# Kernel tuning notes

Hardware: AMD Instinct MI355X
Metric: run time of the kernel (lower is better)

The kernel has to match this reference:

```python
import jax, jax.numpy as jnp
import numpy as np

N, E, B, H, W = 2048, 65536, 4, 64, 64
D, ED, HID, ATT, STEPS = 128, 128, 256, 16, 4
NODE_IN, EDGE_IN = 256, 64


def setup_inputs() -> dict:
    key = jax.random.key(0)
    ks = jax.random.split(key, 24)
    p = lambda k, s: jax.random.normal(k, s, jnp.float32) * 0.05
    z = lambda n: jnp.zeros((n,), jnp.float32)
    return dict(
        x=jax.random.normal(ks[0], (N, NODE_IN), jnp.float32),
        edge_attr=jax.random.normal(ks[1], (E, EDGE_IN), jnp.float32),
        edge_index=jax.random.randint(ks[2], (2, E), 0, N),
        feature_maps=jax.random.normal(ks[3], (B, 32, H, W), jnp.float32),
        batch_index=jax.random.randint(ks[4], (N,), 0, B),
        ne_w=p(ks[5], (D, NODE_IN)), ne_b=z(D),
        ee_w=p(ks[6], (ED, EDGE_IN)), ee_b=z(ED),
        me_w1=p(ks[7], (HID, 2 * (D + ATT) + ED)), me_b1=z(HID),
        me_w2=p(ks[8], (ED, HID)), me_b2=z(ED),
        mn_w=p(ks[9], (D, D + ATT + ED)), mn_b=z(D),
        key_w=p(ks[10], (ATT, D)), key_b=z(ATT),
        q_w=p(ks[11], (ATT, 32)), q_b=z(ATT),
        v_w=p(ks[12], (ATT, 32)), v_b=z(ATT),
        ec_w1=p(ks[13], (64, ED)), ec_b1=z(64),
        ec_w2=p(ks[14], (1, 64)), ec_b2=z(1),
        nc_w1=p(ks[15], (64, D)), nc_b1=z(64),
        nc_w2=p(ks[16], (1, 64)), nc_b2=z(1),
        cl_w1=p(ks[17], (64, D)), cl_b1=z(64),
        cl_w2=p(ks[18], (17, 64)), cl_b2=z(17),
    )


def _forward(x, edge_attr, feature_maps, edge_index, batch_index,
             ne_w, ne_b, ee_w, ee_b, me_w1, me_b1, me_w2, me_b2, mn_w, mn_b,
             key_w, key_b, q_w, q_b, v_w, v_b,
             ec_w1, ec_b1, ec_w2, ec_b2, nc_w1, nc_b1, nc_w2, nc_b2,
             cl_w1, cl_b1, cl_w2, cl_b2):
    relu = jax.nn.relu
    node_features = relu(x @ ne_w.T + ne_b)            # [N, D]
    edge_features = relu(edge_attr @ ee_w.T + ee_b)    # [E, ED]
    fm = feature_maps.reshape(B, 32, H * W)
    queries = jnp.einsum('oc,bcp->bop', q_w, fm) + q_b[None, :, None]  # [B,ATT,HW]
    values = jnp.einsum('oc,bcp->bop', v_w, fm) + v_b[None, :, None]   # [B,ATT,HW]
    src, tgt = edge_index[0], edge_index[1]  # j, i (messages aggregated at i)
    node_ids = jnp.arange(N)
    for _ in range(STEPS):
        k = node_features @ key_w.T + key_b                        # [N, ATT]
        attn = jax.nn.softmax(jnp.einsum('nk,bkp->bnp', k, queries), axis=2)
        result = jnp.einsum('bkp,bnp->bkn', values, attn)          # [B, ATT, N]
        res = result[batch_index, :, node_ids]                     # [N, ATT]
        nf = jnp.concatenate([node_features, res], axis=1)         # [N, D+ATT]
        x_i, x_j = nf[tgt], nf[src]
        edge_features = relu(relu(jnp.concatenate([x_i, x_j, edge_features], 1) @ me_w1.T + me_b1) @ me_w2.T + me_b2)
        msg = relu(jnp.concatenate([x_i, edge_features], 1) @ mn_w.T + mn_b)
        node_features = jax.ops.segment_sum(msg, tgt, num_segments=N)
    pe = (relu(edge_features @ ec_w1.T + ec_b1) @ ec_w2.T + ec_b2).squeeze(-1)
    pn = (relu(node_features @ nc_w1.T + nc_b1) @ nc_w2.T + nc_b2).squeeze(-1)
    pc = relu(node_features @ cl_w1.T + cl_b1) @ cl_w2.T + cl_b2
    return pe, pn, pc, node_features, edge_features


def reference(x, edge_attr, edge_index, feature_maps, batch_index,
              ne_w, ne_b, ee_w, ee_b, me_w1, me_b1, me_w2, me_b2, mn_w, mn_b,
              key_w, key_b, q_w, q_b, v_w, v_b,
              ec_w1, ec_b1, ec_w2, ec_b2, nc_w1, nc_b1, nc_w2, nc_b2,
              cl_w1, cl_b1, cl_w2, cl_b2):
    return _forward(x, edge_attr, feature_maps, edge_index, batch_index,
                    ne_w, ne_b, ee_w, ee_b, me_w1, me_b1, me_w2, me_b2, mn_w, mn_b,
                    key_w, key_b, q_w, q_b, v_w, v_b,
                    ec_w1, ec_b1, ec_w2, ec_b2, nc_w1, nc_b1, nc_w2, nc_b2,
                    cl_w1, cl_b1, cl_w2, cl_b2)
```

## Files before the change

### kernel.cpp

```cpp
#include <hip/hip_runtime.h>

#define N_NODES 2048
#define N_EDGES 65536
#define BATCH   4
#define PPIX    4096
#define STEPS   4

typedef __attribute__((ext_vector_type(4))) float f32x4;
typedef __attribute__((ext_vector_type(8))) short s16x8;

__device__ __forceinline__ unsigned short f2bf(float f) {
    unsigned u = __float_as_uint(f);
    unsigned r = u + 0x7fffu + ((u >> 16) & 1u);
    return (unsigned short)(r >> 16);
}
__device__ __forceinline__ float bf2f(unsigned short h) {
    return __uint_as_float(((unsigned)h) << 16);
}

__global__ __launch_bounds__(256) void k_hist(const int* __restrict__ ei,
                                              const int* __restrict__ batch_ix,
                                              int* __restrict__ hist,
                                              int* __restrict__ bcnt) {
    int i = blockIdx.x * 256 + threadIdx.x;
    if (i < N_EDGES) atomicAdd(&hist[ei[N_EDGES + i]], 1);
    if (i < N_NODES) atomicAdd(&bcnt[batch_ix[i]], 1);
}

__global__ __launch_bounds__(256) void k_scan(const int* __restrict__ hist,
                                              const int* __restrict__ bcnt,
                                              int* __restrict__ cursor,
                                              int* __restrict__ boff,
                                              int* __restrict__ bcur) {
    __shared__ int tls[256];
    const int t = threadIdx.x;
    int loc[8];
    int s = 0;
#pragma unroll
    for (int j = 0; j < 8; j++) { loc[j] = s; s += hist[t * 8 + j]; }
    tls[t] = s;
    __syncthreads();
    for (int off = 1; off < 256; off <<= 1) {
        int v = (t >= off) ? tls[t - off] : 0;
        __syncthreads();
        tls[t] += v;
        __syncthreads();
    }
    int base = (t > 0) ? tls[t - 1] : 0;
#pragma unroll
    for (int j = 0; j < 8; j++) cursor[t * 8 + j] = base + loc[j];
    if (t == 0) {
        int b = 0;
        for (int i = 0; i < 4; i++) { boff[i] = b; bcur[i] = b; b += bcnt[i]; }
    }
}

__global__ __launch_bounds__(256) void k_scatter(const int* __restrict__ ei,
                                                 const int* __restrict__ batch_ix,
                                                 int* __restrict__ cursor, int* __restrict__ bcur,
                                                 int* __restrict__ perm, int* __restrict__ nperm) {
    int i = blockIdx.x * 256 + threadIdx.x;
    if (i < N_EDGES) {
        int pos = atomicAdd(&cursor[ei[N_EDGES + i]], 1);
        perm[pos] = i;
    }
    if (i < N_NODES) {
        int pos = atomicAdd(&bcur[batch_ix[i]], 1);
        nperm[pos] = i;
    }
}

__global__ void k_wconv(const float* __restrict__ w1, const float* __restrict__ w2,
                        const float* __restrict__ w3, const float* __restrict__ ec1,
                        const float* __restrict__ eew, const float* __restrict__ new_,
                        unsigned short* __restrict__ o1, unsigned short* __restrict__ o2,
                        unsigned short* __restrict__ o3, unsigned short* __restrict__ o4,
                        unsigned short* __restrict__ o5, unsigned short* __restrict__ o6) {
    int i = blockIdx.x * 256 + threadIdx.x;
    if (i < 256 * 416) o1[i] = f2bf(w1[i]);
    if (i < 128 * 256) o2[i] = f2bf(w2[i]);
    if (i < 128 * 288) {
        int r = i / 288, c = i - r * 288;
        o3[i] = (c < 272) ? f2bf(w3[r * 272 + c]) : (unsigned short)0;
    }
    if (i < 64 * 128) o4[i] = f2bf(ec1[i]);
    if (i < 128 * 64) o5[i] = f2bf(eew[i]);
    if (i < 128 * 256) o6[i] = f2bf(new_[i]);
}

__global__ __launch_bounds__(256) void k_node_enc(const float* __restrict__ x,
                                                  const unsigned short* __restrict__ wb,
                                                  const float* __restrict__ b,
                                                  float* __restrict__ out) {
    __shared__ __attribute__((aligned(16))) unsigned short xs2[64 * 264];
    const int tid = threadIdx.x;
    const int n0 = blockIdx.x * 64;
    {
        int row = tid >> 2, qq = tid & 3;
        const float* rp = x + (size_t)(n0 + row) * 256 + qq * 64;
        unsigned short* dp = &xs2[row * 264 + qq * 64];
#pragma unroll
        for (int j = 0; j < 4; j++) {
            float4 f0 = *(const float4*)(rp + j * 16 + 0);
            float4 f1 = *(const float4*)(rp + j * 16 + 4);
            float4 f2 = *(const float4*)(rp + j * 16 + 8);
            float4 f3 = *(const float4*)(rp + j * 16 + 12);
            s16x8 lo, hi;
            lo[0] = (short)f2bf(f0.x); lo[1] = (short)f2bf(f0.y); lo[2] = (short)f2bf(f0.z); lo[3] = (short)f2bf(f0.w);
            lo[4] = (short)f2bf(f1.x); lo[5] = (short)f2bf(f1.y); lo[6] = (short)f2bf(f1.z); lo[7] = (short)f2bf(f1.w);
            hi[0] = (short)f2bf(f2.x); hi[1] = (short)f2bf(f2.y); hi[2] = (short)f2bf(f2.z); hi[3] = (short)f2bf(f2.w);
            hi[4] = (short)f2bf(f3.x); hi[5] = (short)f2bf(f3.y); hi[6] = (short)f2bf(f3.z); hi[7] = (short)f2bf(f3.w);
            *(s16x8*)(dp + j * 16) = lo;
            *(s16x8*)(dp + j * 16 + 8) = hi;
        }
    }
    __syncthreads();
    const int lane = tid & 63;
    const int wn = tid >> 6;
    const int lr = lane & 15;
    const int lk = lane >> 4;
    const f32x4 z4 = {0.f, 0.f, 0.f, 0.f};
    f32x4 acc[4][2];
#pragma unroll
    for (int mt = 0; mt < 4; mt++)
#pragma unroll
        for (int nt = 0; nt < 2; nt++) acc[mt][nt] = z4;
#pragma unroll
    for (int kc = 0; kc < 8; kc++) {
        s16x8 a0 = *(const s16x8*)&xs2[(0 + lr) * 264 + kc * 32 + lk * 8];
        s16x8 a1 = *(const s16x8*)&xs2[(16 + lr) * 264 + kc * 32 + lk * 8];
        s16x8 a2 = *(const s16x8*)&xs2[(32 + lr) * 264 + kc * 32 + lk * 8];
        s16x8 a3 = *(const s16x8*)&xs2[(48 + lr) * 264 + kc * 32 + lk * 8];
#pragma unroll
        for (int nt = 0; nt < 2; nt++) {
            int nn = wn * 32 + nt * 16 + lr;
            s16x8 bf = *(const s16x8*)&wb[(size_t)nn * 256 + kc * 32 + lk * 8];
            acc[0][nt] = __builtin_amdgcn_mfma_f32_16x16x32_bf16(a0, bf, acc[0][nt], 0, 0, 0);
            acc[1][nt] = __builtin_amdgcn_mfma_f32_16x16x32_bf16(a1, bf, acc[1][nt], 0, 0, 0);
            acc[2][nt] = __builtin_amdgcn_mfma_f32_16x16x32_bf16(a2, bf, acc[2][nt], 0, 0, 0);
            acc[3][nt] = __builtin_amdgcn_mfma_f32_16x16x32_bf16(a3, bf, acc[3][nt], 0, 0, 0);
        }
    }
#pragma unroll
    for (int nt = 0; nt < 2; nt++) {
        int nn = wn * 32 + nt * 16 + lr;
        float bias = b[nn];
#pragma unroll
        for (int mt = 0; mt < 4; mt++)
#pragma unroll
            for (int r = 0; r < 4; r++) {
                int m = mt * 16 + lk * 4 + r;
                out[(size_t)(n0 + m) * 128 + nn] = fmaxf(acc[mt][nt][r] + bias, 0.f);
            }
    }
}

__global__ __launch_bounds__(256) void k_edge_enc(const float* __restrict__ ea,
                                                  const unsigned short* __restrict__ wb,
                                                  const float* __restrict__ b,
                                                  const int* __restrict__ perm,
                                                  unsigned short* __restrict__ ef) {
    __shared__ __attribute__((aligned(16))) unsigned short eas[64 * 72];
    __shared__ int ep[64];
    const int tid = threadIdx.x;
    const int e0 = blockIdx.x * 64;
    if (tid < 64) ep[tid] = perm[e0 + tid];
    __syncthreads();
    {
        int row = tid >> 2, qq = tid & 3;
        const float* rp = ea + (size_t)ep[row] * 64 + qq * 16;
        float4 f0 = *(const float4*)(rp + 0);
        float4 f1 = *(const float4*)(rp + 4);
        float4 f2 = *(const float4*)(rp + 8);
        float4 f3 = *(const float4*)(rp + 12);
        s16x8 lo, hi;
        lo[0] = (short)f2bf(f0.x); lo[1] = (short)f2bf(f0.y); lo[2] = (short)f2bf(f0.z); lo[3] = (short)f2bf(f0.w);
        lo[4] = (short)f2bf(f1.x); lo[5] = (short)f2bf(f1.y); lo[6] = (short)f2bf(f1.z); lo[7] = (short)f2bf(f1.w);
        hi[0] = (short)f2bf(f2.x); hi[1] = (short)f2bf(f2.y); hi[2] = (short)f2bf(f2.z); hi[3] = (short)f2bf(f2.w);
        hi[4] = (short)f2bf(f3.x); hi[5] = (short)f2bf(f3.y); hi[6] = (short)f2bf(f3.z); hi[7] = (short)f2bf(f3.w);
        unsigned short* dp = &eas[row * 72 + qq * 16];
        *(s16x8*)(dp) = lo;
        *(s16x8*)(dp + 8) = hi;
    }
    __syncthreads();
    const int lane = tid & 63;
    const int wn = tid >> 6;
    const int lr = lane & 15;
    const int lk = lane >> 4;
    const f32x4 z4 = {0.f, 0.f, 0.f, 0.f};
    f32x4 acc[4][2];
#pragma unroll
    for (int mt = 0; mt < 4; mt++)
#pragma unroll
        for (int nt = 0; nt < 2; nt++) acc[mt][nt] = z4;
#pragma unroll
    for (int kc = 0; kc < 2; kc++) {
        s16x8 a0 = *(const s16x8*)&eas[(0 + lr) * 72 + kc * 32 + lk * 8];
        s16x8 a1 = *(const s16x8*)&eas[(16 + lr) * 72 + kc * 32 + lk * 8];
        s16x8 a2 = *(const s16x8*)&eas[(32 + lr) * 72 + kc * 32 + lk * 8];
        s16x8 a3 = *(const s16x8*)&eas[(48 + lr) * 72 + kc * 32 + lk * 8];
#pragma unroll
        for (int nt = 0; nt < 2; nt++) {
            int nn = wn * 32 + nt * 16 + lr;
            s16x8 bf = *(const s16x8*)&wb[(size_t)nn * 64 + kc * 32 + lk * 8];
            acc[0][nt] = __builtin_amdgcn_mfma_f32_16x16x32_bf16(a0, bf, acc[0][nt], 0, 0, 0);
            acc[1][nt] = __builtin_amdgcn_mfma_f32_16x16x32_bf16(a1, bf, acc[1][nt], 0, 0, 0);
            acc[2][nt] = __builtin_amdgcn_mfma_f32_16x16x32_bf16(a2, bf, acc[2][nt], 0, 0, 0);
            acc[3][nt] = __builtin_amdgcn_mfma_f32_16x16x32_bf16(a3, bf, acc[3][nt], 0, 0, 0);
        }
    }
#pragma unroll
    for (int nt = 0; nt < 2; nt++) {
        int nn = wn * 32 + nt * 16 + lr;
        float bias = b[nn];
#pragma unroll
        for (int mt = 0; mt < 4; mt++)
#pragma unroll
            for (int r = 0; r < 4; r++) {
                int m = mt * 16 + lk * 4 + r;
                ef[(size_t)(e0 + m) * 128 + nn] = f2bf(fmaxf(acc[mt][nt][r] + bias, 0.f));
            }
    }
}

__global__ __launch_bounds__(256) void k_qv(const float* __restrict__ fm,
                                            const float* __restrict__ qw, const float* __restrict__ qb,
                                            const float* __restrict__ vw, const float* __restrict__ vb,
                                            float* __restrict__ q, float* __restrict__ v) {
    __shared__ float fs[32][256];
    const int b = blockIdx.x >> 4;
    const int pt = blockIdx.x & 15;
    for (int i = threadIdx.x; i < 32 * 256; i += 256) {
        int c = i >> 8, p = i & 255;
        fs[c][p] = fm[(size_t)b * 32 * PPIX + (size_t)c * PPIX + pt * 256 + p];
    }
    __syncthreads();
    const int p = threadIdx.x;
    for (int o = 0; o < 16; o++) {
        float qa = qb[o], va = vb[o];
#pragma unroll
        for (int c = 0; c < 32; c++) {
            float f = fs[c][p];
            qa += qw[o * 32 + c] * f;
            va += vw[o * 32 + c] * f;
        }
        size_t oidx = ((size_t)b * 16 + o) * PPIX + pt * 256 + p;
        q[oidx] = qa;
        v[oidx] = va;
    }
}

__global__ __launch_bounds__(256) void k_attn(const float* __restrict__ nf,
                                              const float* __restrict__ qbuf,
                                              const float* __restrict__ vbuf,
                                              const float* __restrict__ key_w,
                                              const float* __restrict__ key_b,
                                              const int* __restrict__ nperm,
                                              const int* __restrict__ boff,
                                              const int* __restrict__ bcnt,
                                              unsigned short* __restrict__ nf_bf,
                                              float* __restrict__ nxt) {
    const int b = blockIdx.x >> 9;
    const int chunk = blockIdx.x & 511;
    const int cnt = bcnt[b];
    if (chunk * 4 >= cnt) return;
    const int base = boff[b] + chunk * 4;
    const int nvalid = min(4, cnt - chunk * 4);
    const int t = threadIdx.x;

    __shared__ int nid[4];
    __shared__ float xs[4][128];
    __shared__ float ks[4][16];
    __shared__ float redm[4][4];
    __shared__ float pbuf[4][4][17];

    if (t < 4) nid[t] = nperm[base + ((t < nvalid) ? t : 0)];
    __syncthreads();
    for (int i2 = t; i2 < 4 * 128; i2 += 256) {
        int i = i2 >> 7, d = i2 & 127;
        xs[i][d] = nf[(size_t)nid[i] * 128 + d];
        if (i < nvalid) nxt[(size_t)nid[i] * 128 + d] = 0.f;
    }
    __syncthreads();
    if (t < 64) {
        int i = t >> 4, a = t & 15;
        const float* wr = key_w + a * 128;
        float acc = key_b[a];
#pragma unroll 8
        for (int c = 0; c < 128; c++) acc += xs[i][c] * wr[c];
        ks[i][a] = acc;
    }
    __syncthreads();
    float kk[4][16];
#pragma unroll
    for (int i = 0; i < 4; i++)
#pragma unroll
        for (int a = 0; a < 16; a++) kk[i][a] = ks[i][a];

    const float* q = qbuf + (size_t)b * 16 * PPIX;
    const float* v = vbuf + (size_t)b * 16 * PPIX;

    float s[4][16];
    float m[4] = {-3e38f, -3e38f, -3e38f, -3e38f};
#pragma unroll
    for (int ch = 0; ch < 16; ch++) {
        int p = ch * 256 + t;
        float qv[16];
#pragma unroll
        for (int a = 0; a < 16; a++) qv[a] = q[a * PPIX + p];
#pragma unroll
        for (int i = 0; i < 4; i++) {
            float acc = 0.f;
#pragma unroll
            for (int a = 0; a < 16; a++) acc += kk[i][a] * qv[a];
            s[i][ch] = acc;
            m[i] = fmaxf(m[i], acc);
        }
    }
#pragma unroll
    for (int off = 1; off < 64; off <<= 1)
#pragma unroll
        for (int i = 0; i < 4; i++) m[i] = fmaxf(m[i], __shfl_xor(m[i], off));
    const int wv = t >> 6;
    if ((t & 63) == 0) {
#pragma unroll
        for (int i = 0; i < 4; i++) redm[wv][i] = m[i];
    }
    __syncthreads();
    float mf[4];
#pragma unroll
    for (int i = 0; i < 4; i++)
        mf[i] = fmaxf(fmaxf(redm[0][i], redm[1][i]), fmaxf(redm[2][i], redm[3][i]));

    float wsm[4] = {0.f, 0.f, 0.f, 0.f};
    float vacc[4][16];
#pragma unroll
    for (int i = 0; i < 4; i++)
#pragma unroll
        for (int a = 0; a < 16; a++) vacc[i][a] = 0.f;
#pragma unroll
    for (int ch = 0; ch < 16; ch++) {
        int p = ch * 256 + t;
        float vv[16];
#pragma unroll
        for (int a = 0; a < 16; a++) vv[a] = v[a * PPIX + p];
#pragma unroll
        for (int i = 0; i < 4; i++) {
            float w = __expf(s[i][ch] - mf[i]);
            wsm[i] += w;
#pragma unroll
            for (int a = 0; a < 16; a++) vacc[i][a] += w * vv[a];
        }
    }
#pragma unroll
    for (int off = 1; off < 64; off <<= 1)
#pragma unroll
        for (int i = 0; i < 4; i++) {
            wsm[i] += __shfl_xor(wsm[i], off);
#pragma unroll
            for (int a = 0; a < 16; a++) vacc[i][a] += __shfl_xor(vacc[i][a], off);
        }
    if ((t & 63) == 0) {
#pragma unroll
        for (int i = 0; i < 4; i++) {
            pbuf[wv][i][0] = wsm[i];
#pragma unroll
            for (int a = 0; a < 16; a++) pbuf[wv][i][1 + a] = vacc[i][a];
        }
    }
    __syncthreads();
    if (t < 64) {
        int i = t >> 4, a = t & 15;
        float den = pbuf[0][i][0] + pbuf[1][i][0] + pbuf[2][i][0] + pbuf[3][i][0];
        float num = pbuf[0][i][1 + a] + pbuf[1][i][1 + a] + pbuf[2][i][1 + a] + pbuf[3][i][1 + a];
        if (i < nvalid) nf_bf[(size_t)nid[i] * 144 + 128 + a] = f2bf(num / den);
    }
    for (int i2 = t; i2 < 4 * 128; i2 += 256) {
        int i = i2 >> 7, d = i2 & 127;
        if (i < nvalid) nf_bf[(size_t)nid[i] * 144 + d] = f2bf(xs[i][d]);
    }
}

__global__ __launch_bounds__(512, 2) void k_mlp(const unsigned short* __restrict__ nf_bf,
                                                unsigned short* __restrict__ ef_buf,
                                                const unsigned short* __restrict__ w1b,
                                                const unsigned short* __restrict__ w2b,
                                                const unsigned short* __restrict__ w3b,
                                                const float* __restrict__ me_b1,
                                                const float* __restrict__ me_b2,
                                                const float* __restrict__ mn_b,
                                                const int* __restrict__ ei,
                                                const int* __restrict__ perm,
                                                float* __restrict__ node_acc) {
    __shared__ __attribute__((aligned(16))) unsigned short catA[128 * 424];
    __shared__ int tgt_s[128];
    __shared__ int src_s[128];
    const int tid = threadIdx.x;
    const int e0 = blockIdx.x * 128;
    const int* srcI = ei;
    const int* tgtI = ei + N_EDGES;
    if (tid < 128) {
        int eg = perm[e0 + tid];
        tgt_s[tid] = tgtI[eg];
        src_s[tid] = srcI[eg];
    }
    __syncthreads();
    for (int c = tid; c < 128 * 52; c += 512) {
        int e = c / 52;
        int r = c - e * 52;
        const unsigned short* sp;
        int dcol;
        if (r < 18)      { sp = nf_bf + (size_t)tgt_s[e] * 144 + r * 8;        dcol = r * 8; }
        else if (r < 36) { sp = nf_bf + (size_t)src_s[e] * 144 + (r - 18) * 8; dcol = 144 + (r - 18) * 8; }
        else             { sp = ef_buf + (size_t)(e0 + e) * 128 + (r - 36) * 8; dcol = 288 + (r - 36) * 8; }
        *(s16x8*)&catA[e * 424 + dcol] = *(const s16x8*)sp;
    }
    __syncthreads();

    const int lane = tid & 63;
    const int wn = tid >> 6;
    const int lr = lane & 15;
    const int lk = lane >> 4;
    const f32x4 z4 = {0.f, 0.f, 0.f, 0.f};

    f32x4 acc[8][2];
#pragma unroll
    for (int mt = 0; mt < 8; mt++)
#pragma unroll
        for (int nt = 0; nt < 2; nt++) acc[mt][nt] = z4;
#pragma unroll 2
    for (int kc = 0; kc < 13; kc++) {
        s16x8 a0 = *(const s16x8*)&catA[(0 * 16 + lr) * 424 + kc * 32 + lk * 8];
        s16x8 a1 = *(const s16x8*)&catA[(1 * 16 + lr) * 424 + kc * 32 + lk * 8];
        s16x8 a2 = *(const s16x8*)&catA[(2 * 16 + lr) * 424 + kc * 32 + lk * 8];
        s16x8 a3 = *(const s16x8*)&catA[(3 * 16 + lr) * 424 + kc * 32 + lk * 8];
        s16x8 a4 = *(const s16x8*)&catA[(4 * 16 + lr) * 424 + kc * 32 + lk * 8];
        s16x8 a5 = *(const s16x8*)&catA[(5 * 16 + lr) * 424 + kc * 32 + lk * 8];
        s16x8 a6 = *(const s16x8*)&catA[(6 * 16 + lr) * 424 + kc * 32 + lk * 8];
        s16x8 a7 = *(const s16x8*)&catA[(7 * 16 + lr) * 424 + kc * 32 + lk * 8];
#pragma unroll
        for (int nt = 0; nt < 2; nt++) {
            int nn = wn * 32 + nt * 16 + lr;
            s16x8 b = *(const s16x8*)&w1b[(size_t)nn * 416 + kc * 32 + lk * 8];
            acc[0][nt] = __builtin_amdgcn_mfma_f32_16x16x32_bf16(a0, b, acc[0][nt], 0, 0, 0);
            acc[1][nt] = __builtin_amdgcn_mfma_f32_16x16x32_bf16(a1, b, acc[1][nt], 0, 0, 0);
            acc[2][nt] = __builtin_amdgcn_mfma_f32_16x16x32_bf16(a2, b, acc[2][nt], 0, 0, 0);
            acc[3][nt] = __builtin_amdgcn_mfma_f32_16x16x32_bf16(a3, b, acc[3][nt], 0, 0, 0);
            acc[4][nt] = __builtin_amdgcn_mfma_f32_16x16x32_bf16(a4, b, acc[4][nt], 0, 0, 0);
            acc[5][nt] = __builtin_amdgcn_mfma_f32_16x16x32_bf16(a5, b, acc[5][nt], 0, 0, 0);
            acc[6][nt] = __builtin_amdgcn_mfma_f32_16x16x32_bf16(a6, b, acc[6][nt], 0, 0, 0);
            acc[7][nt] = __builtin_amdgcn_mfma_f32_16x16x32_bf16(a7, b, acc[7][nt], 0, 0, 0);
        }
    }
    __syncthreads();
#pragma unroll
    for (int nt = 0; nt < 2; nt++) {
        int nn = wn * 32 + nt * 16 + lr;
        float bias = me_b1[nn];
#pragma unroll
        for (int mt = 0; mt < 8; mt++)
#pragma unroll
            for (int r = 0; r < 4; r++) {
                int m = mt * 16 + lk * 4 + r;
                catA[m * 424 + 144 + nn] = f2bf(fmaxf(acc[mt][nt][r] + bias, 0.f));
            }
    }
    __syncthreads();

    f32x4 acc2[8];
#pragma unroll
    for (int mt = 0; mt < 8; mt++) acc2[mt] = z4;
    const int nn2 = wn * 16 + lr;
#pragma unroll 2
    for (int kc = 0; kc < 8; kc++) {
        s16x8 a0 = *(const s16x8*)&catA[(0 * 16 + lr) * 424 + 144 + kc * 32 + lk * 8];
        s16x8 a1 = *(const s16x8*)&catA[(1 * 16 + lr) * 424 + 144 + kc * 32 + lk * 8];
        s16x8 a2 = *(const s16x8*)&catA[(2 * 16 + lr) * 424 + 144 + kc * 32 + lk * 8];
        s16x8 a3 = *(const s16x8*)&catA[(3 * 16 + lr) * 424 + 144 + kc * 32 + lk * 8];
        s16x8 a4 = *(const s16x8*)&catA[(4 * 16 + lr) * 424 + 144 + kc * 32 + lk * 8];
        s16x8 a5 = *(const s16x8*)&catA[(5 * 16 + lr) * 424 + 144 + kc * 32 + lk * 8];
        s16x8 a6 = *(const s16x8*)&catA[(6 * 16 + lr) * 424 + 144 + kc * 32 + lk * 8];
        s16x8 a7 = *(const s16x8*)&catA[(7 * 16 + lr) * 424 + 144 + kc * 32 + lk * 8];
        s16x8 b = *(const s16x8*)&w2b[(size_t)nn2 * 256 + kc * 32 + lk * 8];
        acc2[0] = __builtin_amdgcn_mfma_f32_16x16x32_bf16(a0, b, acc2[0], 0, 0, 0);
        acc2[1] = __builtin_amdgcn_mfma_f32_16x16x32_bf16(a1, b, acc2[1], 0, 0, 0);
        acc2[2] = __builtin_amdgcn_mfma_f32_16x16x32_bf16(a2, b, acc2[2], 0, 0, 0);
        acc2[3] = __builtin_amdgcn_mfma_f32_16x16x32_bf16(a3, b, acc2[3], 0, 0, 0);
        acc2[4] = __builtin_amdgcn_mfma_f32_16x16x32_bf16(a4, b, acc2[4], 0, 0, 0);
        acc2[5] = __builtin_amdgcn_mfma_f32_16x16x32_bf16(a5, b, acc2[5], 0, 0, 0);
        acc2[6] = __builtin_amdgcn_mfma_f32_16x16x32_bf16(a6, b, acc2[6], 0, 0, 0);
        acc2[7] = __builtin_amdgcn_mfma_f32_16x16x32_bf16(a7, b, acc2[7], 0, 0, 0);
    }
    __syncthreads();
#pragma unroll
    for (int mt = 0; mt < 8; mt++)
#pragma unroll
        for (int r = 0; r < 4; r++) {
            int m = mt * 16 + lk * 4 + r;
            catA[m * 424 + 144 + nn2] = f2bf(fmaxf(acc2[mt][r] + me_b2[nn2], 0.f));
        }
    __syncthreads();

    f32x4 acc3[8];
#pragma unroll
    for (int mt = 0; mt < 8; mt++) acc3[mt] = z4;
#pragma unroll 2
    for (int kc = 0; kc < 9; kc++) {
        s16x8 a0 = *(const s16x8*)&catA[(0 * 16 + lr) * 424 + kc * 32 + lk * 8];
        s16x8 a1 = *(const s16x8*)&catA[(1 * 16 + lr) * 424 + kc * 32 + lk * 8];
        s16x8 a2 = *(const s16x8*)&catA[(2 * 16 + lr) * 424 + kc * 32 + lk * 8];
        s16x8 a3 = *(const s16x8*)&catA[(3 * 16 + lr) * 424 + kc * 32 + lk * 8];
        s16x8 a4 = *(const s16x8*)&catA[(4 * 16 + lr) * 424 + kc * 32 + lk * 8];
        s16x8 a5 = *(const s16x8*)&catA[(5 * 16 + lr) * 424 + kc * 32 + lk * 8];
        s16x8 a6 = *(const s16x8*)&catA[(6 * 16 + lr) * 424 + kc * 32 + lk * 8];
        s16x8 a7 = *(const s16x8*)&catA[(7 * 16 + lr) * 424 + kc * 32 + lk * 8];
        s16x8 b = *(const s16x8*)&w3b[(size_t)nn2 * 288 + kc * 32 + lk * 8];
        acc3[0] = __builtin_amdgcn_mfma_f32_16x16x32_bf16(a0, b, acc3[0], 0, 0, 0);
        acc3[1] = __builtin_amdgcn_mfma_f32_16x16x32_bf16(a1, b, acc3[1], 0, 0, 0);
        acc3[2] = __builtin_amdgcn_mfma_f32_16x16x32_bf16(a2, b, acc3[2], 0, 0, 0);
        acc3[3] = __builtin_amdgcn_mfma_f32_16x16x32_bf16(a3, b, acc3[3], 0, 0, 0);
        acc3[4] = __builtin_amdgcn_mfma_f32_16x16x32_bf16(a4, b, acc3[4], 0, 0, 0);
        acc3[5] = __builtin_amdgcn_mfma_f32_16x16x32_bf16(a5, b, acc3[5], 0, 0, 0);
        acc3[6] = __builtin_amdgcn_mfma_f32_16x16x32_bf16(a6, b, acc3[6], 0, 0, 0);
        acc3[7] = __builtin_amdgcn_mfma_f32_16x16x32_bf16(a7, b, acc3[7], 0, 0, 0);
    }
    __syncthreads();
#pragma unroll
    for (int mt = 0; mt < 8; mt++)
#pragma unroll
        for (int r = 0; r < 4; r++) {
            int m = mt * 16 + lk * 4 + r;
            *(float*)&catA[m * 424 + 144 + nn2 * 2] = fmaxf(acc3[mt][r] + mn_b[nn2], 0.f);
        }
    __syncthreads();
    {
        const int c = tid & 127;
        const int r0 = (tid >> 7) * 32;
        float run = *(const float*)&catA[r0 * 424 + 144 + c * 2];
        int prev = tgt_s[r0];
        for (int r = r0 + 1; r < r0 + 32; r++) {
            int tg = tgt_s[r];
            float val = *(const float*)&catA[r * 424 + 144 + c * 2];
            if (tg != prev) {
                atomicAdd(&node_acc[(size_t)prev * 128 + c], run);
                run = val;
                prev = tg;
            } else {
                run += val;
            }
        }
        atomicAdd(&node_acc[(size_t)prev * 128 + c], run);
    }
    {
        float bias = me_b2[nn2];
#pragma unroll
        for (int mt = 0; mt < 8; mt++)
#pragma unroll
            for (int r = 0; r < 4; r++) {
                int m = mt * 16 + lk * 4 + r;
                ef_buf[(size_t)(e0 + m) * 128 + nn2] = f2bf(fmaxf(acc2[mt][r] + bias, 0.f));
            }
    }
}

__global__ __launch_bounds__(256) void k_edge_head(const unsigned short* __restrict__ ef,
                                                   const unsigned short* __restrict__ w1b,
                                                   const float* __restrict__ b1,
                                                   const float* __restrict__ w2,
                                                   const float* __restrict__ b2,
                                                   const int* __restrict__ perm,
                                                   float* __restrict__ pe,
                                                   float* __restrict__ ef_out) {
    __shared__ __attribute__((aligned(16))) unsigned short efs[32][136];
    __shared__ float h_s[32][68];
    __shared__ int ep_s[32];
    const int tid = threadIdx.x;
    const int e0 = blockIdx.x * 32;
    if (tid < 32) ep_s[tid] = perm[e0 + tid];
    __syncthreads();
    for (int c = tid; c < 32 * 16; c += 256) {
        int e = c >> 4, r = c & 15;
        s16x8 v = *(const s16x8*)&ef[(size_t)(e0 + e) * 128 + r * 8];
        *(s16x8*)&efs[e][r * 8] = v;
        float4 lo, hi;
        lo.x = bf2f((unsigned short)v[0]); lo.y = bf2f((unsigned short)v[1]);
        lo.z = bf2f((unsigned short)v[2]); lo.w = bf2f((unsigned short)v[3]);
        hi.x = bf2f((unsigned short)v[4]); hi.y = bf2f((unsigned short)v[5]);
        hi.z = bf2f((unsigned short)v[6]); hi.w = bf2f((unsigned short)v[7]);
        size_t ob = (size_t)ep_s[e] * 128 + r * 8;
        *(float4*)&ef_out[ob] = lo;
        *(float4*)&ef_out[ob + 4] = hi;
    }
    __syncthreads();
    const int lane = tid & 63;
    const int wid = tid >> 6;
    const int lr = lane & 15;
    const int lk = lane >> 4;
    const f32x4 z4 = {0.f, 0.f, 0.f, 0.f};
    f32x4 acc0 = z4, acc1 = z4;
    for (int kc = 0; kc < 4; kc++) {
        s16x8 a0 = *(const s16x8*)&efs[lr][kc * 32 + lk * 8];
        s16x8 a1 = *(const s16x8*)&efs[16 + lr][kc * 32 + lk * 8];
        s16x8 b = *(const s16x8*)&w1b[(size_t)(wid * 16 + lr) * 128 + kc * 32 + lk * 8];
        acc0 = __builtin_amdgcn_mfma_f32_16x16x32_bf16(a0, b, acc0, 0, 0, 0);
        acc1 = __builtin_amdgcn_mfma_f32_16x16x32_bf16(a1, b, acc1, 0, 0, 0);
    }
    {
        int h = wid * 16 + lr;
        float bias = b1[h];
#pragma unroll
        for (int r = 0; r < 4; r++) {
            h_s[lk * 4 + r][h]      = fmaxf(acc0[r] + bias, 0.f);
            h_s[16 + lk * 4 + r][h] = fmaxf(acc1[r] + bias, 0.f);
        }
    }
    __syncthreads();
    if (tid < 32) {
        float a = b2[0];
#pragma unroll 8
        for (int h = 0; h < 64; h++) a += w2[h] * h_s[tid][h];
        pe[ep_s[tid]] = a;
    }
}

__global__ __launch_bounds__(64) void k_node_heads(const float* __restrict__ nf,
                                                   const float* __restrict__ nc_w1, const float* __restrict__ nc_b1,
                                                   const float* __restrict__ nc_w2, const float* __restrict__ nc_b2,
                                                   const float* __restrict__ cl_w1, const float* __restrict__ cl_b1,
                                                   const float* __restrict__ cl_w2, const float* __restrict__ cl_b2,
                                                   float* __restrict__ pn, float* __restrict__ pc,
                                                   float* __restrict__ nf_out) {
    __shared__ float xs[128];
    __shared__ float hr2[64];
    const int n = blockIdx.x;
    const int t = threadIdx.x;
    float2 xv = *(const float2*)&nf[(size_t)n * 128 + t * 2];
    xs[t * 2] = xv.x;
    xs[t * 2 + 1] = xv.y;
    *(float2*)&nf_out[(size_t)n * 128 + t * 2] = xv;
    __syncthreads();
    float a1 = nc_b1[t], a2 = cl_b1[t];
#pragma unroll 8
    for (int d4 = 0; d4 < 32; d4++) {
        float4 w1v = *(const float4*)&nc_w1[(size_t)t * 128 + d4 * 4];
        float4 w2v = *(const float4*)&cl_w1[(size_t)t * 128 + d4 * 4];
        float x0 = xs[d4 * 4], x1 = xs[d4 * 4 + 1], x2 = xs[d4 * 4 + 2], x3 = xs[d4 * 4 + 3];
        a1 += x0 * w1v.x + x1 * w1v.y + x2 * w1v.z + x3 * w1v.w;
        a2 += x0 * w2v.x + x1 * w2v.y + x2 * w2v.z + x3 * w2v.w;
    }
    float h1 = fmaxf(a1, 0.f);
    hr2[t] = fmaxf(a2, 0.f);
    float p = nc_w2[t] * h1;
#pragma unroll
    for (int off = 32; off > 0; off >>= 1) p += __shfl_down(p, off);
    if (t == 0) pn[n] = p + nc_b2[0];
    __syncthreads();
    if (t < 17) {
        float a = cl_b2[t];
#pragma unroll 8
        for (int h = 0; h < 64; h++) a += cl_w2[t * 64 + h] * hr2[h];
        pc[(size_t)n * 17 + t] = a;
    }
}

extern "C" void kernel_launch(void* const* d_in, const int* in_sizes, int n_in,
                              void* d_out, int out_size, void* d_ws, size_t ws_size,
                              hipStream_t stream) {
    const float* x         = (const float*)d_in[0];
    const float* edge_attr = (const float*)d_in[1];
    const int*   edge_idx  = (const int*)d_in[2];
    const float* fmaps     = (const float*)d_in[3];
    const int*   batch_ix  = (const int*)d_in[4];
    const float* ne_w  = (const float*)d_in[5];
    const float* ne_b  = (const float*)d_in[6];
    const float* ee_w  = (const float*)d_in[7];
    const float* ee_b  = (const float*)d_in[8];
    const float* me_w1 = (const float*)d_in[9];
    const float* me_b1 = (const float*)d_in[10];
    const float* me_w2 = (const float*)d_in[11];
    const float* me_b2 = (const float*)d_in[12];
    const float* mn_w  = (const float*)d_in[13];
    const float* mn_b  = (const float*)d_in[14];
    const float* key_w = (const float*)d_in[15];
    const float* key_b = (const float*)d_in[16];
    const float* q_w   = (const float*)d_in[17];
    const float* q_b   = (const float*)d_in[18];
    const float* v_w   = (const float*)d_in[19];
    const float* v_b   = (const float*)d_in[20];
    const float* ec_w1 = (const float*)d_in[21];
    const float* ec_b1 = (const float*)d_in[22];
    const float* ec_w2 = (const float*)d_in[23];
    const float* ec_b2 = (const float*)d_in[24];
    const float* nc_w1 = (const float*)d_in[25];
    const float* nc_b1 = (const float*)d_in[26];
    const float* nc_w2 = (const float*)d_in[27];
    const float* nc_b2 = (const float*)d_in[28];
    const float* cl_w1 = (const float*)d_in[29];
    const float* cl_b1 = (const float*)d_in[30];
    const float* cl_w2 = (const float*)d_in[31];
    const float* cl_b2 = (const float*)d_in[32];

    char* wsp = (char*)d_ws;
    size_t off = 0;
    auto alloc = [&](size_t bytes) -> void* {
        void* p = wsp + off;
        off += (bytes + 255) & ~(size_t)255;
        return p;
    };
    float* q_buf = (float*)alloc((size_t)BATCH * 16 * PPIX * sizeof(float));
    float* v_buf = (float*)alloc((size_t)BATCH * 16 * PPIX * sizeof(float));
    float* nfA   = (float*)alloc((size_t)N_NODES * 128 * sizeof(float));
    float* nfB   = (float*)alloc((size_t)N_NODES * 128 * sizeof(float));
    unsigned short* nf_bf  = (unsigned short*)alloc((size_t)N_NODES * 144 * 2);
    unsigned short* ef_buf = (unsigned short*)alloc((size_t)N_EDGES * 128 * 2);
    unsigned short* w1b = (unsigned short*)alloc(256 * 416 * 2);
    unsigned short* w2b = (unsigned short*)alloc(128 * 256 * 2);
    unsigned short* w3b = (unsigned short*)alloc(128 * 288 * 2);
    unsigned short* w4b = (unsigned short*)alloc(64 * 128 * 2);
    unsigned short* w5b = (unsigned short*)alloc(128 * 64 * 2);
    unsigned short* w6b = (unsigned short*)alloc(128 * 256 * 2);
    int* hist   = (int*)alloc((2048 + 4) * sizeof(int));
    int* bcnt   = hist + 2048;
    int* cursor = (int*)alloc(2048 * sizeof(int));
    int* boff   = (int*)alloc(4 * sizeof(int));
    int* bcur   = (int*)alloc(4 * sizeof(int));
    int* perm   = (int*)alloc((size_t)N_EDGES * sizeof(int));
    int* nperm  = (int*)alloc((size_t)N_NODES * sizeof(int));

    float* pe_out = (float*)d_out;
    float* pn_out = pe_out + N_EDGES;
    float* pc_out = pn_out + N_NODES;
    float* nf_out = pc_out + (size_t)N_NODES * 17;
    float* ef_out = nf_out + (size_t)N_NODES * 128;

    hipMemsetAsync(hist, 0, (2048 + 4) * sizeof(int), stream);
    k_hist<<<N_EDGES / 256, 256, 0, stream>>>(edge_idx, batch_ix, hist, bcnt);
    k_scan<<<1, 256, 0, stream>>>(hist, bcnt, cursor, boff, bcur);
    k_scatter<<<N_EDGES / 256, 256, 0, stream>>>(edge_idx, batch_ix, cursor, bcur, perm, nperm);

    k_wconv<<<416, 256, 0, stream>>>(me_w1, me_w2, mn_w, ec_w1, ee_w, ne_w,
                                     w1b, w2b, w3b, w4b, w5b, w6b);
    k_node_enc<<<N_NODES / 64, 256, 0, stream>>>(x, w6b, ne_b, nfA);
    k_qv<<<64, 256, 0, stream>>>(fmaps, q_w, q_b, v_w, v_b, q_buf, v_buf);
    k_edge_enc<<<N_EDGES / 64, 256, 0, stream>>>(edge_attr, w5b, ee_b, perm, ef_buf);

    float* cur = nfA;
    float* nxt = nfB;
    for (int step = 0; step < STEPS; step++) {
        k_attn<<<BATCH * 512, 256, 0, stream>>>(cur, q_buf, v_buf, key_w, key_b,
                                                nperm, boff, bcnt, nf_bf, nxt);
        k_mlp<<<N_EDGES / 128, 512, 0, stream>>>(nf_bf, ef_buf, w1b, w2b, w3b,
                                                 me_b1, me_b2, mn_b, edge_idx, perm, nxt);
        float* tmp = cur; cur = nxt; nxt = tmp;
    }

    k_edge_head<<<N_EDGES / 32, 256, 0, stream>>>(ef_buf, w4b, ec_b1, ec_w2, ec_b2, perm, pe_out, ef_out);
    k_node_heads<<<N_NODES, 64, 0, stream>>>(cur, nc_w1, nc_b1, nc_w2, nc_b2,
                                             cl_w1, cl_b1, cl_w2, cl_b2, pn_out, pc_out, nf_out);
}
```

Baseline: 669.5 us.

## Split attention over pixel quarters with merge kernel and bf16 pixel-major Q/V

Q and V are now stored in bf16, pixel-major with 16 attention channels contiguous, so each thread loads them as vectors instead of strided fp32 reads. The attention kernel is split into four partial blocks per node group, each covering a quarter of the pixels and writing its partial max, denominator and numerator. A new merge kernel combines the partials with a log-sum-exp rescale, writes nf_bf and zeroes nxt. This gives four times more blocks and fewer registers per thread, at the cost of an extra launch, a partials buffer and reduced Q/V precision.

```diff
diff --git a/kernel.cpp b/kernel.cpp
--- a/kernel.cpp
+++ b/kernel.cpp
@@ -226,7 +226,7 @@
 __global__ __launch_bounds__(256) void k_qv(const float* __restrict__ fm,
                                             const float* __restrict__ qw, const float* __restrict__ qb,
                                             const float* __restrict__ vw, const float* __restrict__ vb,
-                                            float* __restrict__ q, float* __restrict__ v) {
+                                            unsigned short* __restrict__ qt_, unsigned short* __restrict__ vt_) {
     __shared__ float fs[32][256];
     const int b = blockIdx.x >> 4;
     const int pt = blockIdx.x & 15;
@@ -236,32 +236,45 @@
     }
     __syncthreads();
     const int p = threadIdx.x;
+    float qa[16], va[16];
+#pragma unroll
     for (int o = 0; o < 16; o++) {
-        float qa = qb[o], va = vb[o];
+        float qv = qb[o], vv = vb[o];
 #pragma unroll
         for (int c = 0; c < 32; c++) {
             float f = fs[c][p];
-            qa += qw[o * 32 + c] * f;
-            va += vw[o * 32 + c] * f;
-        }
-        size_t oidx = ((size_t)b * 16 + o) * PPIX + pt * 256 + p;
-        q[oidx] = qa;
-        v[oidx] = va;
-    }
-}
-
-__global__ __launch_bounds__(256) void k_attn(const float* __restrict__ nf,
-                                              const float* __restrict__ qbuf,
-                                              const float* __restrict__ vbuf,
-                                              const float* __restrict__ key_w,
-                                              const float* __restrict__ key_b,
-                                              const int* __restrict__ nperm,
-                                              const int* __restrict__ boff,
-                                              const int* __restrict__ bcnt,
-                                              unsigned short* __restrict__ nf_bf,
-                                              float* __restrict__ nxt) {
-    const int b = blockIdx.x >> 9;
-    const int chunk = blockIdx.x & 511;
+            qv += qw[o * 32 + c] * f;
+            vv += vw[o * 32 + c] * f;
+        }
+        qa[o] = qv;
+        va[o] = vv;
+    }
+    s16x8 q0, q1, v0, v1;
+#pragma unroll
+    for (int j = 0; j < 8; j++) {
+        q0[j] = (short)f2bf(qa[j]);     q1[j] = (short)f2bf(qa[8 + j]);
+        v0[j] = (short)f2bf(va[j]);     v1[j] = (short)f2bf(va[8 + j]);
+    }
+    size_t base = ((size_t)b * PPIX + pt * 256 + p) * 16;
+    *(s16x8*)&qt_[base] = q0;
+    *(s16x8*)&qt_[base + 8] = q1;
+    *(s16x8*)&vt_[base] = v0;
+    *(s16x8*)&vt_[base + 8] = v1;
+}
+
+__global__ __launch_bounds__(256) void k_attn_part(const float* __restrict__ nf,
+                                                   const unsigned short* __restrict__ qt_,
+                                                   const unsigned short* __restrict__ vt_,
+                                                   const float* __restrict__ key_w,
+                                                   const float* __restrict__ key_b,
+                                                   const int* __restrict__ nperm,
+                                                   const int* __restrict__ boff,
+                                                   const int* __restrict__ bcnt,
+                                                   float* __restrict__ parts) {
+    const int b = blockIdx.x >> 11;
+    const int rem = blockIdx.x & 2047;
+    const int chunk = rem >> 2;
+    const int qt = rem & 3;
     const int cnt = bcnt[b];
     if (chunk * 4 >= cnt) return;
     const int base = boff[b] + chunk * 4;
@@ -279,7 +292,6 @@
     for (int i2 = t; i2 < 4 * 128; i2 += 256) {
         int i = i2 >> 7, d = i2 & 127;
         xs[i][d] = nf[(size_t)nid[i] * 128 + d];
-        if (i < nvalid) nxt[(size_t)nid[i] * 128 + d] = 0.f;
     }
     __syncthreads();
     if (t < 64) {
@@ -297,17 +309,22 @@
 #pragma unroll
         for (int a = 0; a < 16; a++) kk[i][a] = ks[i][a];
 
-    const float* q = qbuf + (size_t)b * 16 * PPIX;
-    const float* v = vbuf + (size_t)b * 16 * PPIX;
-
-    float s[4][16];
+    const unsigned short* qp = qt_ + ((size_t)b * PPIX + qt * 1024) * 16;
+    const unsigned short* vp = vt_ + ((size_t)b * PPIX + qt * 1024) * 16;
+
+    float s[4][4];
     float m[4] = {-3e38f, -3e38f, -3e38f, -3e38f};
 #pragma unroll
-    for (int ch = 0; ch < 16; ch++) {
+    for (int ch = 0; ch < 4; ch++) {
         int p = ch * 256 + t;
+        s16x8 qlo = *(const s16x8*)&qp[(size_t)p * 16];
+        s16x8 qhi = *(const s16x8*)&qp[(size_t)p * 16 + 8];
         float qv[16];
 #pragma unroll
-        for (int a = 0; a < 16; a++) qv[a] = q[a * PPIX + p];
+        for (int j = 0; j < 8; j++) {
+            qv[j] = bf2f((unsigned short)qlo[j]);
+            qv[8 + j] = bf2f((unsigned short)qhi[j]);
+        }
 #pragma unroll
         for (int i = 0; i < 4; i++) {
             float acc = 0.f;
@@ -339,11 +356,16 @@
 #pragma unroll
         for (int a = 0; a < 16; a++) vacc[i][a] = 0.f;
 #pragma unroll
-    for (int ch = 0; ch < 16; ch++) {
+    for (int ch = 0; ch < 4; ch++) {
         int p = ch * 256 + t;
+        s16x8 vlo = *(const s16x8*)&vp[(size_t)p * 16];
+        s16x8 vhi = *(const s16x8*)&vp[(size_t)p * 16 + 8];
         float vv[16];
 #pragma unroll
-        for (int a = 0; a < 16; a++) vv[a] = v[a * PPIX + p];
+        for (int j = 0; j < 8; j++) {
+            vv[j] = bf2f((unsigned short)vlo[j]);
+            vv[8 + j] = bf2f((unsigned short)vhi[j]);
+        }
 #pragma unroll
         for (int i = 0; i < 4; i++) {
             float w = __expf(s[i][ch] - mf[i]);
@@ -373,11 +395,33 @@
         int i = t >> 4, a = t & 15;
         float den = pbuf[0][i][0] + pbuf[1][i][0] + pbuf[2][i][0] + pbuf[3][i][0];
         float num = pbuf[0][i][1 + a] + pbuf[1][i][1 + a] + pbuf[2][i][1 + a] + pbuf[3][i][1 + a];
-        if (i < nvalid) nf_bf[(size_t)nid[i] * 144 + 128 + a] = f2bf(num / den);
-    }
-    for (int i2 = t; i2 < 4 * 128; i2 += 256) {
-        int i = i2 >> 7, d = i2 & 127;
-        if (i < nvalid) nf_bf[(size_t)nid[i] * 144 + d] = f2bf(xs[i][d]);
+        if (i < nvalid) {
+            float* pp = &parts[((size_t)nid[i] * 4 + qt) * 18];
+            if (a == 0) { pp[0] = mf[i]; pp[1] = den; }
+            pp[2 + a] = num;
+        }
+    }
+}
+
+__global__ __launch_bounds__(256) void k_attn_merge(const float* __restrict__ nf,
+                                                    const float* __restrict__ parts,
+                                                    unsigned short* __restrict__ nf_bf,
+                                                    float* __restrict__ nxt) {
+    const int nb0 = blockIdx.x * 16;
+    const int t = threadIdx.x;
+    const int i = t >> 4, a = t & 15;
+    const int n = nb0 + i;
+    const float* pp = &parts[(size_t)n * 72];
+    float m0 = pp[0], m1 = pp[18], m2 = pp[36], m3 = pp[54];
+    float mg = fmaxf(fmaxf(m0, m1), fmaxf(m2, m3));
+    float e0 = __expf(m0 - mg), e1 = __expf(m1 - mg), e2 = __expf(m2 - mg), e3 = __expf(m3 - mg);
+    float den = pp[1] * e0 + pp[19] * e1 + pp[37] * e2 + pp[55] * e3;
+    float num = pp[2 + a] * e0 + pp[20 + a] * e1 + pp[38 + a] * e2 + pp[56 + a] * e3;
+    nf_bf[(size_t)n * 144 + 128 + a] = f2bf(num / den);
+    for (int j = t; j < 16 * 128; j += 256) {
+        int n2 = nb0 + (j >> 7), d = j & 127;
+        nf_bf[(size_t)n2 * 144 + d] = f2bf(nf[(size_t)n2 * 128 + d]);
+        nxt[(size_t)n2 * 128 + d] = 0.f;
     }
 }
 
@@ -707,8 +751,9 @@
         off += (bytes + 255) & ~(size_t)255;
         return p;
     };
-    float* q_buf = (float*)alloc((size_t)BATCH * 16 * PPIX * sizeof(float));
-    float* v_buf = (float*)alloc((size_t)BATCH * 16 * PPIX * sizeof(float));
+    unsigned short* q_buf = (unsigned short*)alloc((size_t)BATCH * PPIX * 16 * 2);
+    unsigned short* v_buf = (unsigned short*)alloc((size_t)BATCH * PPIX * 16 * 2);
+    float* parts = (float*)alloc((size_t)N_NODES * 4 * 18 * sizeof(float));
     float* nfA   = (float*)alloc((size_t)N_NODES * 128 * sizeof(float));
     float* nfB   = (float*)alloc((size_t)N_NODES * 128 * sizeof(float));
     unsigned short* nf_bf  = (unsigned short*)alloc((size_t)N_NODES * 144 * 2);
@@ -747,8 +792,9 @@
     float* cur = nfA;
     float* nxt = nfB;
     for (int step = 0; step < STEPS; step++) {
-        k_attn<<<BATCH * 512, 256, 0, stream>>>(cur, q_buf, v_buf, key_w, key_b,
-                                                nperm, boff, bcnt, nf_bf, nxt);
+        k_attn_part<<<BATCH * 2048, 256, 0, stream>>>(cur, q_buf, v_buf, key_w, key_b,
+                                                      nperm, boff, bcnt, parts);
+        k_attn_merge<<<N_NODES / 16, 256, 0, stream>>>(cur, parts, nf_bf, nxt);
         k_mlp<<<N_EDGES / 128, 512, 0, stream>>>(nf_bf, ef_buf, w1b, w2b, w3b,
                                                  me_b1, me_b2, mn_b, edge_idx, perm, nxt);
         float* tmp = cur; cur = nxt; nxt = tmp;
```

Measured after the change: 676.4 us. Within noise of the previous version (+1.0%).
